# Optimization experiments

Hardware: AMD Instinct MI355X
Metric: run time of the kernel (lower is better)

## Reference

```python
import jax, jax.numpy as jnp
import numpy as np

B, T, E, H = 4, 2048, 1024, 16
D = E // H  # head_dim = 64
THETA = 10000.0


def setup_inputs() -> dict:
    key = jax.random.key(0)
    ks = jax.random.split(key, 3)
    s = 0.02
    return {
        "x": jax.random.normal(ks[0], (B, T, E), jnp.float32),
        "W_attn": jax.random.normal(ks[1], (E, 3 * E), jnp.float32) * s,
        "b_attn": jnp.zeros((3 * E,), jnp.float32),
        "W_proj": jax.random.normal(ks[2], (E, E), jnp.float32) * s,
        "b_proj": jnp.zeros((E,), jnp.float32),
    }


def _rope(x, position_offset=0):
    # x: (B, H, T, D) -- interleaved even/odd pair rotation, as in apply_rope
    t, d = x.shape[2], x.shape[3]
    pos = jnp.arange(position_offset, position_offset + t, dtype=jnp.float32)
    inv_freq = 1.0 / (THETA ** (jnp.arange(0, d, 2, dtype=jnp.float32) / d))
    freqs = jnp.outer(pos, inv_freq)  # (T, D/2)
    cos = jnp.cos(freqs)[None, None].astype(x.dtype)
    sin = jnp.sin(freqs)[None, None].astype(x.dtype)
    xe = x[..., ::2]
    xo = x[..., 1::2]
    rot = jnp.stack((xe * cos - xo * sin, xe * sin + xo * cos), axis=-1)
    return rot.reshape(x.shape)


def reference(x, W_attn, b_attn, W_proj, b_proj):
    # fused qkv projection
    qkv = x @ W_attn + b_attn  # (B, T, 3E)
    q, k, v = jnp.split(qkv, 3, axis=-1)

    def heads(a):
        return a.reshape(B, T, H, D).transpose(0, 2, 1, 3)  # (B,H,T,D)

    q, k, v = heads(q), heads(k), heads(v)
    q = _rope(q)
    k = _rope(k)

    scores = jnp.einsum('bhqd,bhkd->bhqk', q, k) * (D ** -0.5)  # (B,H,T,T)
    causal = jnp.tril(jnp.ones((T, T), dtype=bool))
    scores = jnp.where(causal[None, None], scores, -jnp.inf)
    weights = jax.nn.softmax(scores, axis=-1)  # dropout p=0 (eval) -> identity

    out = jnp.einsum('bhqk,bhkd->bhqd', weights, v)
    out = out.transpose(0, 2, 1, 3).reshape(B, T, E)
    return out @ W_proj + b_proj
```

## Files before the change

kernel.cpp:

```cpp
#include <hip/hip_runtime.h>
#include <hip/hip_bf16.h>
#include <math.h>

#define TT 2048
#define HH 16

typedef short s16x8 __attribute__((ext_vector_type(8)));
typedef float f32x4 __attribute__((ext_vector_type(4)));

#define F4(p) (*reinterpret_cast<const float4*>(p))

__device__ __forceinline__ void gload16(const void* g, void* l) {
    __builtin_amdgcn_global_load_lds(
        (const __attribute__((address_space(1))) void*)g,
        (__attribute__((address_space(3))) void*)l, 16, 0, 0);
}

__device__ __forceinline__ ushort bf1(float a) {
    __hip_bfloat16 h = __float2bfloat16(a);
    union { __hip_bfloat16 h1; ushort u; } c; c.h1 = h; return c.u;
}
__device__ __forceinline__ uint pack_bf2(float a, float b) {
    __hip_bfloat162 h = __float22bfloat162_rn(make_float2(a, b));
    union { __hip_bfloat162 h2; uint u; } c; c.h2 = h; return c.u;
}

__global__ void rope_table_kernel(float2* __restrict__ cs) {
    int idx = blockIdx.x * 256 + threadIdx.x;
    int t = idx >> 5;
    int i = idx & 31;
    double inv_d = exp(((double)(-2 * i) / 64.0) * log(10000.0));
    float invf = (float)inv_d;
    float freq = (float)t * invf;
    double df = (double)freq;
    cs[idx] = make_float2((float)cos(df), (float)sin(df));
}

__global__ __launch_bounds__(256) void convert_f32_bf16(const float* __restrict__ in,
                                                        ushort* __restrict__ out) {
    size_t i = (size_t)(blockIdx.x * 256 + threadIdx.x) * 8;
    float4 a = F4(&in[i]); float4 b = F4(&in[i + 4]);
    s16x8 v;
    v[0] = bf1(a.x); v[1] = bf1(a.y); v[2] = bf1(a.z); v[3] = bf1(a.w);
    v[4] = bf1(b.x); v[5] = bf1(b.y); v[6] = bf1(b.z); v[7] = bf1(b.w);
    *reinterpret_cast<s16x8*>(&out[i]) = v;
}

__global__ __launch_bounds__(256) void transpose_f32_bf16(const float* __restrict__ in,
                                                          ushort* __restrict__ out,
                                                          int R, int C) {
    __shared__ float t[64][65];
    int r0 = blockIdx.y * 64, c0 = blockIdx.x * 64;
    int ix = threadIdx.x & 15, iy = threadIdx.x >> 4;
#pragma unroll
    for (int j = 0; j < 4; ++j) {
        float4 v = F4(&in[(size_t)(r0 + iy + j * 16) * C + c0 + ix * 4]);
        t[iy + j * 16][ix * 4 + 0] = v.x;
        t[iy + j * 16][ix * 4 + 1] = v.y;
        t[iy + j * 16][ix * 4 + 2] = v.z;
        t[iy + j * 16][ix * 4 + 3] = v.w;
    }
    __syncthreads();
    int oc = threadIdx.x >> 2, seg = threadIdx.x & 3;
    s16x8 u0, u1;
#pragma unroll
    for (int i = 0; i < 8; ++i) u0[i] = bf1(t[seg * 16 + i][oc]);
#pragma unroll
    for (int i = 0; i < 8; ++i) u1[i] = bf1(t[seg * 16 + 8 + i][oc]);
    ushort* dst = &out[(size_t)(c0 + oc) * R + r0 + seg * 16];
    *reinterpret_cast<s16x8*>(dst) = u0;
    *reinterpret_cast<s16x8*>(dst + 8) = u1;
}

__global__ __launch_bounds__(256, 2) void qkv_gemm_kernel(
    const ushort* __restrict__ xb,
    const ushort* __restrict__ wat,
    const float* __restrict__ bias,
    const float2* __restrict__ cs,
    ushort* __restrict__ qg, ushort* __restrict__ kg, ushort* __restrict__ vt)
{
    __shared__ ushort As[2][8192];
    __shared__ ushort Bs[2][8192];

    const int tid = threadIdx.x;
    const int lane = tid & 63, wid = tid >> 6;
    const int lane15 = lane & 15, kgrp = lane >> 4;
    const int wr = wid >> 1, wc = wid & 1;
    const int m0 = blockIdx.y * 128, n0 = blockIdx.x * 128;
    const int swz = (lane15 & 7) << 4;
    const int srcsw = ((lane & 7) ^ ((lane >> 3) & 7)) * 8;
    const int kgrp16 = kgrp * 16;
    const float SCL = 0.125f * 1.44269504088896f;

    f32x4 acc[4][4] = {};

#define STAGE_QKV(bufi, kofs)                                                     \
    do {                                                                          \
        _Pragma("unroll")                                                         \
        for (int i_ = 0; i_ < 4; ++i_) {                                          \
            int c_ = wid * 4 + i_;                                                \
            gload16(xb + (size_t)(m0 + c_ * 8 + (lane >> 3)) * 1024 + (kofs) + srcsw, \
                    &As[bufi][c_ * 512]);                                         \
            gload16(wat + (size_t)(n0 + c_ * 8 + (lane >> 3)) * 1024 + (kofs) + srcsw, \
                    &Bs[bufi][c_ * 512]);                                         \
        }                                                                         \
    } while (0)

    STAGE_QKV(0, 0);
    int buf = 0;
    for (int kt = 0; kt < 16; ++kt) {
        __syncthreads();
        if (kt < 15) STAGE_QKV(buf ^ 1, (kt + 1) * 64);
        const char* Ap = (const char*)As[buf];
        const char* Bp = (const char*)Bs[buf];
#pragma unroll
        for (int ks = 0; ks < 2; ++ks) {
            s16x8 af[4], bfv[4];
            const int kb = (ks * 64 + kgrp16) ^ swz;
#pragma unroll
            for (int f = 0; f < 4; ++f) {
                int row = wr * 64 + f * 16 + lane15;
                af[f] = *reinterpret_cast<const s16x8*>(Ap + row * 128 + kb);
            }
#pragma unroll
            for (int g = 0; g < 4; ++g) {
                int row = wc * 64 + g * 16 + lane15;
                bfv[g] = *reinterpret_cast<const s16x8*>(Bp + row * 128 + kb);
            }
            __builtin_amdgcn_s_setprio(1);
#pragma unroll
            for (int f = 0; f < 4; ++f)
#pragma unroll
                for (int g = 0; g < 4; ++g)
                    acc[f][g] = __builtin_amdgcn_mfma_f32_16x16x32_bf16(
                        af[f], bfv[g], acc[f][g], 0, 0, 0);
            __builtin_amdgcn_s_setprio(0);
        }
        buf ^= 1;
    }

#pragma unroll
    for (int g = 0; g < 4; ++g) {
        const int n = n0 + wc * 64 + g * 16 + lane15;
        const int sec = n >> 10;
        const int e = n & 1023;
        const int hh = e >> 6, d = e & 63;
        const float bsv = bias[n];
#pragma unroll
        for (int f = 0; f < 4; ++f) {
            const int mb = m0 + wr * 64 + f * 16 + kgrp * 4;
            const int bb = mb >> 11;
            const int t0 = mb & 2047;
            if (sec == 2) {
                float v0 = acc[f][g][0] + bsv, v1 = acc[f][g][1] + bsv;
                float v2 = acc[f][g][2] + bsv, v3 = acc[f][g][3] + bsv;
                uint2 u = make_uint2(pack_bf2(v0, v1), pack_bf2(v2, v3));
                *reinterpret_cast<uint2*>(
                    &vt[((size_t)(bb * HH + hh) * 64 + d) * TT + t0]) = u;
            } else {
                ushort* dst = (sec == 0) ? qg : kg;
#pragma unroll
                for (int r = 0; r < 4; ++r) {
                    float v = acc[f][g][r] + bsv;
                    float p = __shfl_xor(v, 1);
                    float2 c2 = cs[(t0 + r) * 32 + (d >> 1)];
                    float rv = (d & 1) ? (p * c2.y + v * c2.x) : (v * c2.x - p * c2.y);
                    if (sec == 0) rv *= SCL;
                    dst[((size_t)(bb * HH + hh) * TT + t0 + r) * 64 + d] = bf1(rv);
                }
            }
        }
    }
#undef STAGE_QKV
}

__global__ __launch_bounds__(512, 4) void flash_kernel(
    const ushort* __restrict__ qg, const ushort* __restrict__ kg,
    const ushort* __restrict__ vt, ushort* __restrict__ aob)
{
    __shared__ ushort Q_s[8192];
    __shared__ ushort K_s[2][4096];
    __shared__ ushort V_s[2][4096];
    __shared__ ushort P_s[8192];

    const int tid = threadIdx.x;
    const int lane = tid & 63, wid = tid >> 6;
    const int lane15 = lane & 15, kgrp = lane >> 4;
    const int j = blockIdx.x;
    const int qt = 15 - (j >> 6);
    const int bh = j & 63;
    const int b = bh >> 4, h = bh & 15;
    const int q0 = qt * 128;
    const int wq = wid * 16;
    const int wq_abs = q0 + wq;
    const int swz = (lane15 & 7) << 4;
    const int srcsw = ((lane & 7) ^ ((lane >> 3) & 7)) * 8;
    const int kgrp16 = kgrp * 16;
    const int nt = 2 * qt + 2;

    const ushort* qp = qg + (size_t)bh * TT * 64;
    const ushort* kp = kg + (size_t)bh * TT * 64;
    const ushort* vp = vt + (size_t)bh * 64 * TT;

#define STAGE_KV(bufi, kv0_)                                                      \
    do {                                                                          \
        gload16(kp + (size_t)((kv0_) + wid * 8 + (lane >> 3)) * 64 + srcsw,       \
                &K_s[bufi][wid * 512]);                                           \
        gload16(vp + (size_t)(wid * 8 + (lane >> 3)) * TT + (kv0_) + srcsw,       \
                &V_s[bufi][wid * 512]);                                           \
    } while (0)

#pragma unroll
    for (int i = 0; i < 2; ++i) {
        int c = wid * 2 + i;
        gload16(qp + (size_t)(q0 + c * 8 + (lane >> 3)) * 64 + srcsw, &Q_s[c * 512]);
    }
    STAGE_KV(0, 0);

    f32x4 o[4] = {};
    float mreg = -3.0e38f;
    float lreg = 0.f;

    int buf = 0;
    for (int t = 0; t < nt; ++t) {
        __syncthreads();
        if (t + 1 < nt) STAGE_KV(buf ^ 1, (t + 1) * 64);

        const int kv0 = t * 64;
        if (kv0 <= wq_abs + 15) {
            const char* Kp = (const char*)K_s[buf];
            const char* Vp = (const char*)V_s[buf];

            f32x4 sacc[4] = {};
#pragma unroll
            for (int ks = 0; ks < 2; ++ks) {
                const int kb = (ks * 64 + kgrp16) ^ swz;
                s16x8 ka[4], qb;
#pragma unroll
                for (int kf = 0; kf < 4; ++kf)
                    ka[kf] = *reinterpret_cast<const s16x8*>(Kp + (kf * 16 + lane15) * 128 + kb);
                qb = *reinterpret_cast<const s16x8*>((const char*)Q_s + (wq + lane15) * 128 + kb);
                __builtin_amdgcn_s_setprio(1);
#pragma unroll
                for (int kf = 0; kf < 4; ++kf)
                    sacc[kf] = __builtin_amdgcn_mfma_f32_16x16x32_bf16(
                        ka[kf], qb, sacc[kf], 0, 0, 0);
                __builtin_amdgcn_s_setprio(0);
            }

            const int qglob = q0 + wq + lane15;
            const bool masked = (kv0 + 63 > wq_abs);
            float mx = -3.0e38f;
            if (masked) {
#pragma unroll
                for (int kf = 0; kf < 4; ++kf)
#pragma unroll
                    for (int r = 0; r < 4; ++r) {
                        int kvg = kv0 + kf * 16 + kgrp * 4 + r;
                        float v = (kvg > qglob) ? -3.0e38f : sacc[kf][r];
                        sacc[kf][r] = v;
                        mx = fmaxf(mx, v);
                    }
            } else {
#pragma unroll
                for (int kf = 0; kf < 4; ++kf)
#pragma unroll
                    for (int r = 0; r < 4; ++r) mx = fmaxf(mx, sacc[kf][r]);
            }
            mx = fmaxf(mx, __shfl_xor(mx, 16));
            mx = fmaxf(mx, __shfl_xor(mx, 32));
            if (!__all(mx <= mreg + 8.f)) {
                const float mnew = fmaxf(mreg, mx);
                const float fs = exp2f(mreg - mnew);
                lreg *= fs;
#pragma unroll
                for (int df = 0; df < 4; ++df) o[df] *= fs;
                mreg = mnew;
            }
            float rsum = 0.f;
            const int prow = wq + lane15;
#pragma unroll
            for (int kf = 0; kf < 4; ++kf) {
                float p0 = exp2f(sacc[kf][0] - mreg);
                float p1 = exp2f(sacc[kf][1] - mreg);
                float p2 = exp2f(sacc[kf][2] - mreg);
                float p3 = exp2f(sacc[kf][3] - mreg);
                rsum += (p0 + p1) + (p2 + p3);
                uint2 u = make_uint2(pack_bf2(p0, p1), pack_bf2(p2, p3));
                int kvb = (kf * 32 + kgrp * 8) ^ swz;
                *reinterpret_cast<uint2*>((char*)P_s + prow * 128 + kvb) = u;
            }
            rsum += __shfl_xor(rsum, 16);
            rsum += __shfl_xor(rsum, 32);
            lreg += rsum;

#pragma unroll
            for (int ks = 0; ks < 2; ++ks) {
                const int kb = (ks * 64 + kgrp16) ^ swz;
                s16x8 va[4], pb;
#pragma unroll
                for (int df = 0; df < 4; ++df)
                    va[df] = *reinterpret_cast<const s16x8*>(Vp + (df * 16 + lane15) * 128 + kb);
                pb = *reinterpret_cast<const s16x8*>((const char*)P_s + (wq + lane15) * 128 + kb);
                __builtin_amdgcn_s_setprio(1);
#pragma unroll
                for (int df = 0; df < 4; ++df)
                    o[df] = __builtin_amdgcn_mfma_f32_16x16x32_bf16(
                        va[df], pb, o[df], 0, 0, 0);
                __builtin_amdgcn_s_setprio(0);
            }
        }
        buf ^= 1;
    }

    {
        const float inv = 1.0f / lreg;
        const int row = wq + lane15;
#pragma unroll
        for (int df = 0; df < 4; ++df) {
            float p0 = o[df][0] * inv, p1 = o[df][1] * inv;
            float p2 = o[df][2] * inv, p3 = o[df][3] * inv;
            uint2 u = make_uint2(pack_bf2(p0, p1), pack_bf2(p2, p3));
            int db = (df * 32 + kgrp * 8) ^ ((row & 7) << 4);
            *reinterpret_cast<uint2*>((char*)P_s + row * 128 + db) = u;
        }
    }
    __syncthreads();
    {
        const int q = tid >> 2, seg = tid & 3;
        ushort* orow = aob + ((size_t)(b * TT + q0 + q)) * 1024 + h * 64 + seg * 16;
        int p0 = (seg * 32) ^ ((q & 7) << 4);
        int p1 = (seg * 32 + 16) ^ ((q & 7) << 4);
        s16x8 v0 = *reinterpret_cast<const s16x8*>((const char*)P_s + q * 128 + p0);
        s16x8 v1 = *reinterpret_cast<const s16x8*>((const char*)P_s + q * 128 + p1);
        *reinterpret_cast<s16x8*>(orow) = v0;
        *reinterpret_cast<s16x8*>(orow + 8) = v1;
    }
#undef STAGE_KV
}

__global__ __launch_bounds__(256, 2) void proj_gemm_kernel(
    const ushort* __restrict__ ab,
    const ushort* __restrict__ wpt,
    const float* __restrict__ bias,
    float* __restrict__ out)
{
    __shared__ ushort As[2][8192];
    __shared__ ushort Bs[2][8192];

    const int tid = threadIdx.x;
    const int lane = tid & 63, wid = tid >> 6;
    const int lane15 = lane & 15, kgrp = lane >> 4;
    const int wr = wid >> 1, wc = wid & 1;
    const int m0 = blockIdx.y * 128, n0 = blockIdx.x * 128;
    const int swz = (lane15 & 7) << 4;
    const int srcsw = ((lane & 7) ^ ((lane >> 3) & 7)) * 8;
    const int kgrp16 = kgrp * 16;

    f32x4 acc[4][4] = {};

#define STAGE_PRJ(bufi, kofs)                                                     \
    do {                                                                          \
        _Pragma("unroll")                                                         \
        for (int i_ = 0; i_ < 4; ++i_) {                                          \
            int c_ = wid * 4 + i_;                                                \
            gload16(ab + (size_t)(m0 + c_ * 8 + (lane >> 3)) * 1024 + (kofs) + srcsw, \
                    &As[bufi][c_ * 512]);                                         \
            gload16(wpt + (size_t)(n0 + c_ * 8 + (lane >> 3)) * 1024 + (kofs) + srcsw, \
                    &Bs[bufi][c_ * 512]);                                         \
        }                                                                         \
    } while (0)

    STAGE_PRJ(0, 0);
    int buf = 0;
    for (int kt = 0; kt < 16; ++kt) {
        __syncthreads();
        if (kt < 15) STAGE_PRJ(buf ^ 1, (kt + 1) * 64);
        const char* Ap = (const char*)As[buf];
        const char* Bp = (const char*)Bs[buf];
#pragma unroll
        for (int ks = 0; ks < 2; ++ks) {
            s16x8 af[4], bfv[4];
            const int kb = (ks * 64 + kgrp16) ^ swz;
#pragma unroll
            for (int f = 0; f < 4; ++f) {
                int row = wr * 64 + f * 16 + lane15;
                af[f] = *reinterpret_cast<const s16x8*>(Ap + row * 128 + kb);
            }
#pragma unroll
            for (int g = 0; g < 4; ++g) {
                int row = wc * 64 + g * 16 + lane15;
                bfv[g] = *reinterpret_cast<const s16x8*>(Bp + row * 128 + kb);
            }
            __builtin_amdgcn_s_setprio(1);
#pragma unroll
            for (int f = 0; f < 4; ++f)
#pragma unroll
                for (int g = 0; g < 4; ++g)
                    acc[f][g] = __builtin_amdgcn_mfma_f32_16x16x32_bf16(
                        af[f], bfv[g], acc[f][g], 0, 0, 0);
            __builtin_amdgcn_s_setprio(0);
        }
        buf ^= 1;
    }

#pragma unroll
    for (int g = 0; g < 4; ++g) {
        const int n = n0 + wc * 64 + g * 16 + lane15;
        const float bv = bias[n];
#pragma unroll
        for (int f = 0; f < 4; ++f)
#pragma unroll
            for (int r = 0; r < 4; ++r) {
                const int m = m0 + wr * 64 + f * 16 + kgrp * 4 + r;
                out[(size_t)m * 1024 + n] = acc[f][g][r] + bv;
            }
    }
#undef STAGE_PRJ
}

extern "C" void kernel_launch(void* const* d_in, const int* in_sizes, int n_in,
                              void* d_out, int out_size, void* d_ws, size_t ws_size,
                              hipStream_t stream) {
    const float* x  = (const float*)d_in[0];
    const float* Wa = (const float*)d_in[1];
    const float* ba = (const float*)d_in[2];
    const float* Wp = (const float*)d_in[3];
    const float* bp = (const float*)d_in[4];
    float* out = (float*)d_out;

    char* ws = (char*)d_ws;
    ushort* xb  = (ushort*)(ws + 0);
    ushort* wat = (ushort*)(ws + 16777216);
    ushort* wpt = (ushort*)(ws + 23068672);
    ushort* qg  = (ushort*)(ws + 25165824);
    ushort* kg  = (ushort*)(ws + 41943040);
    ushort* vtg = (ushort*)(ws + 58720256);
    ushort* aob = (ushort*)(ws + 75497472);
    float2* cs  = (float2*)(ws + 92274688);

    rope_table_kernel<<<dim3(256), dim3(256), 0, stream>>>(cs);
    convert_f32_bf16<<<dim3(4096), dim3(256), 0, stream>>>(x, xb);
    transpose_f32_bf16<<<dim3(48, 16), dim3(256), 0, stream>>>(Wa, wat, 1024, 3072);
    transpose_f32_bf16<<<dim3(16, 16), dim3(256), 0, stream>>>(Wp, wpt, 1024, 1024);
    qkv_gemm_kernel<<<dim3(24, 64), dim3(256), 0, stream>>>(xb, wat, ba, cs, qg, kg, vtg);
    flash_kernel<<<dim3(1024), dim3(512), 0, stream>>>(qg, kg, vtg, aob);
    proj_gemm_kernel<<<dim3(8, 64), dim3(256), 0, stream>>>(aob, Wp != nullptr ? wpt : wpt, bp, out);
}
```

Baseline: 276.5 us.

## Fuse prep kernels into one launch and keep Q fragments in registers

Merges the rope table, x conversion and two weight transposes into a single prep kernel with block-range dispatch, which removes three kernel launches and the gaps between them. In the flash kernel, each wave now loads its Q fragments straight from global memory into registers instead of staging them through LDS, which drops the 16KB Q_s buffer. The launch bound is raised to allow 6 blocks per CU. The smaller LDS footprint should permit higher occupancy, at the cost of holding Q in extra VGPRs under a tighter register budget.

```diff
diff --git a/kernel.cpp b/kernel.cpp
--- a/kernel.cpp
+++ b/kernel.cpp
@@ -25,51 +25,56 @@
     union { __hip_bfloat162 h2; uint u; } c; c.h2 = h; return c.u;
 }
 
-__global__ void rope_table_kernel(float2* __restrict__ cs) {
-    int idx = blockIdx.x * 256 + threadIdx.x;
-    int t = idx >> 5;
-    int i = idx & 31;
-    double inv_d = exp(((double)(-2 * i) / 64.0) * log(10000.0));
-    float invf = (float)inv_d;
-    float freq = (float)t * invf;
-    double df = (double)freq;
-    cs[idx] = make_float2((float)cos(df), (float)sin(df));
-}
-
-__global__ __launch_bounds__(256) void convert_f32_bf16(const float* __restrict__ in,
-                                                        ushort* __restrict__ out) {
-    size_t i = (size_t)(blockIdx.x * 256 + threadIdx.x) * 8;
-    float4 a = F4(&in[i]); float4 b = F4(&in[i + 4]);
-    s16x8 v;
-    v[0] = bf1(a.x); v[1] = bf1(a.y); v[2] = bf1(a.z); v[3] = bf1(a.w);
-    v[4] = bf1(b.x); v[5] = bf1(b.y); v[6] = bf1(b.z); v[7] = bf1(b.w);
-    *reinterpret_cast<s16x8*>(&out[i]) = v;
-}
-
-__global__ __launch_bounds__(256) void transpose_f32_bf16(const float* __restrict__ in,
-                                                          ushort* __restrict__ out,
-                                                          int R, int C) {
-    __shared__ float t[64][65];
-    int r0 = blockIdx.y * 64, c0 = blockIdx.x * 64;
-    int ix = threadIdx.x & 15, iy = threadIdx.x >> 4;
-#pragma unroll
-    for (int j = 0; j < 4; ++j) {
-        float4 v = F4(&in[(size_t)(r0 + iy + j * 16) * C + c0 + ix * 4]);
-        t[iy + j * 16][ix * 4 + 0] = v.x;
-        t[iy + j * 16][ix * 4 + 1] = v.y;
-        t[iy + j * 16][ix * 4 + 2] = v.z;
-        t[iy + j * 16][ix * 4 + 3] = v.w;
-    }
-    __syncthreads();
-    int oc = threadIdx.x >> 2, seg = threadIdx.x & 3;
-    s16x8 u0, u1;
-#pragma unroll
-    for (int i = 0; i < 8; ++i) u0[i] = bf1(t[seg * 16 + i][oc]);
-#pragma unroll
-    for (int i = 0; i < 8; ++i) u1[i] = bf1(t[seg * 16 + 8 + i][oc]);
-    ushort* dst = &out[(size_t)(c0 + oc) * R + r0 + seg * 16];
-    *reinterpret_cast<s16x8*>(dst) = u0;
-    *reinterpret_cast<s16x8*>(dst + 8) = u1;
+__global__ __launch_bounds__(256) void prep_kernel(
+    const float* __restrict__ x, const float* __restrict__ Wa,
+    const float* __restrict__ Wp, ushort* __restrict__ xb,
+    ushort* __restrict__ wat, ushort* __restrict__ wpt, float2* __restrict__ cs)
+{
+    __shared__ float tsh[64][65];
+    const int blk = blockIdx.x;
+    const int tid = threadIdx.x;
+
+    if (blk < 256) {
+        int idx = blk * 256 + tid;
+        int t = idx >> 5;
+        int i = idx & 31;
+        double inv_d = exp(((double)(-2 * i) / 64.0) * log(10000.0));
+        float invf = (float)inv_d;
+        float freq = (float)t * invf;
+        double df = (double)freq;
+        cs[idx] = make_float2((float)cos(df), (float)sin(df));
+    } else if (blk < 4352) {
+        size_t i = (size_t)(blk - 256) * 2048 + (size_t)tid * 8;
+        float4 a = F4(&x[i]); float4 b = F4(&x[i + 4]);
+        s16x8 v;
+        v[0] = bf1(a.x); v[1] = bf1(a.y); v[2] = bf1(a.z); v[3] = bf1(a.w);
+        v[4] = bf1(b.x); v[5] = bf1(b.y); v[6] = bf1(b.z); v[7] = bf1(b.w);
+        *reinterpret_cast<s16x8*>(&xb[i]) = v;
+    } else {
+        const float* in; ushort* out; int R, C, bx, by;
+        if (blk < 5120) { int r = blk - 4352; in = Wa; out = wat; R = 1024; C = 3072; bx = r % 48; by = r / 48; }
+        else            { int r = blk - 5120; in = Wp; out = wpt; R = 1024; C = 1024; bx = r & 15; by = r >> 4; }
+        int r0 = by * 64, c0 = bx * 64;
+        int ix = tid & 15, iy = tid >> 4;
+#pragma unroll
+        for (int j = 0; j < 4; ++j) {
+            float4 v = F4(&in[(size_t)(r0 + iy + j * 16) * C + c0 + ix * 4]);
+            tsh[iy + j * 16][ix * 4 + 0] = v.x;
+            tsh[iy + j * 16][ix * 4 + 1] = v.y;
+            tsh[iy + j * 16][ix * 4 + 2] = v.z;
+            tsh[iy + j * 16][ix * 4 + 3] = v.w;
+        }
+        __syncthreads();
+        int oc = tid >> 2, seg = tid & 3;
+        s16x8 u0, u1;
+#pragma unroll
+        for (int i = 0; i < 8; ++i) u0[i] = bf1(tsh[seg * 16 + i][oc]);
+#pragma unroll
+        for (int i = 0; i < 8; ++i) u1[i] = bf1(tsh[seg * 16 + 8 + i][oc]);
+        ushort* dst = &out[(size_t)(c0 + oc) * R + r0 + seg * 16];
+        *reinterpret_cast<s16x8*>(dst) = u0;
+        *reinterpret_cast<s16x8*>(dst + 8) = u1;
+    }
 }
 
 __global__ __launch_bounds__(256, 2) void qkv_gemm_kernel(
@@ -174,11 +179,10 @@
 #undef STAGE_QKV
 }
 
-__global__ __launch_bounds__(512, 4) void flash_kernel(
+__global__ __launch_bounds__(512, 6) void flash_kernel(
     const ushort* __restrict__ qg, const ushort* __restrict__ kg,
     const ushort* __restrict__ vt, ushort* __restrict__ aob)
 {
-    __shared__ ushort Q_s[8192];
     __shared__ ushort K_s[2][4096];
     __shared__ ushort V_s[2][4096];
     __shared__ ushort P_s[8192];
@@ -201,6 +205,7 @@
     const ushort* qp = qg + (size_t)bh * TT * 64;
     const ushort* kp = kg + (size_t)bh * TT * 64;
     const ushort* vp = vt + (size_t)bh * 64 * TT;
+    char* Pw = (char*)P_s + wid * 2048;
 
 #define STAGE_KV(bufi, kv0_)                                                      \
     do {                                                                          \
@@ -210,11 +215,11 @@
                 &V_s[bufi][wid * 512]);                                           \
     } while (0)
 
-#pragma unroll
-    for (int i = 0; i < 2; ++i) {
-        int c = wid * 2 + i;
-        gload16(qp + (size_t)(q0 + c * 8 + (lane >> 3)) * 64 + srcsw, &Q_s[c * 512]);
-    }
+    const ushort* qrow = qp + (size_t)(q0 + wq + lane15) * 64 + kgrp * 8;
+    s16x8 qfr[2];
+    qfr[0] = *reinterpret_cast<const s16x8*>(qrow);
+    qfr[1] = *reinterpret_cast<const s16x8*>(qrow + 32);
+
     STAGE_KV(0, 0);
 
     f32x4 o[4] = {};
@@ -235,16 +240,15 @@
 #pragma unroll
             for (int ks = 0; ks < 2; ++ks) {
                 const int kb = (ks * 64 + kgrp16) ^ swz;
-                s16x8 ka[4], qb;
+                s16x8 ka[4];
 #pragma unroll
                 for (int kf = 0; kf < 4; ++kf)
                     ka[kf] = *reinterpret_cast<const s16x8*>(Kp + (kf * 16 + lane15) * 128 + kb);
-                qb = *reinterpret_cast<const s16x8*>((const char*)Q_s + (wq + lane15) * 128 + kb);
                 __builtin_amdgcn_s_setprio(1);
 #pragma unroll
                 for (int kf = 0; kf < 4; ++kf)
                     sacc[kf] = __builtin_amdgcn_mfma_f32_16x16x32_bf16(
-                        ka[kf], qb, sacc[kf], 0, 0, 0);
+                        ka[kf], qfr[ks], sacc[kf], 0, 0, 0);
                 __builtin_amdgcn_s_setprio(0);
             }
 
@@ -278,7 +282,6 @@
                 mreg = mnew;
             }
             float rsum = 0.f;
-            const int prow = wq + lane15;
 #pragma unroll
             for (int kf = 0; kf < 4; ++kf) {
                 float p0 = exp2f(sacc[kf][0] - mreg);
@@ -288,7 +291,7 @@
                 rsum += (p0 + p1) + (p2 + p3);
                 uint2 u = make_uint2(pack_bf2(p0, p1), pack_bf2(p2, p3));
                 int kvb = (kf * 32 + kgrp * 8) ^ swz;
-                *reinterpret_cast<uint2*>((char*)P_s + prow * 128 + kvb) = u;
+                *reinterpret_cast<uint2*>(Pw + lane15 * 128 + kvb) = u;
             }
             rsum += __shfl_xor(rsum, 16);
             rsum += __shfl_xor(rsum, 32);
@@ -301,7 +304,7 @@
 #pragma unroll
                 for (int df = 0; df < 4; ++df)
                     va[df] = *reinterpret_cast<const s16x8*>(Vp + (df * 16 + lane15) * 128 + kb);
-                pb = *reinterpret_cast<const s16x8*>((const char*)P_s + (wq + lane15) * 128 + kb);
+                pb = *reinterpret_cast<const s16x8*>(Pw + lane15 * 128 + kb);
                 __builtin_amdgcn_s_setprio(1);
 #pragma unroll
                 for (int df = 0; df < 4; ++df)
@@ -439,11 +442,8 @@
     ushort* aob = (ushort*)(ws + 75497472);
     float2* cs  = (float2*)(ws + 92274688);
 
-    rope_table_kernel<<<dim3(256), dim3(256), 0, stream>>>(cs);
-    convert_f32_bf16<<<dim3(4096), dim3(256), 0, stream>>>(x, xb);
-    transpose_f32_bf16<<<dim3(48, 16), dim3(256), 0, stream>>>(Wa, wat, 1024, 3072);
-    transpose_f32_bf16<<<dim3(16, 16), dim3(256), 0, stream>>>(Wp, wpt, 1024, 1024);
+    prep_kernel<<<dim3(5376), dim3(256), 0, stream>>>(x, Wa, Wp, xb, wat, wpt, cs);
     qkv_gemm_kernel<<<dim3(24, 64), dim3(256), 0, stream>>>(xb, wat, ba, cs, qg, kg, vtg);
     flash_kernel<<<dim3(1024), dim3(512), 0, stream>>>(qg, kg, vtg, aob);
-    proj_gemm_kernel<<<dim3(8, 64), dim3(256), 0, stream>>>(aob, Wp != nullptr ? wpt : wpt, bp, out);
-}
+    proj_gemm_kernel<<<dim3(8, 64), dim3(256), 0, stream>>>(aob, wpt, bp, out);
+}
```

After: 270.3 us. 2.2% less time.
